# Kernel tuning notes

Measured on AMD Instinct MI355X. Metric: run time of the kernel, lower is better.

## Reference

```python
import jax, jax.numpy as jnp
import numpy as np
import math

B, S, D, H, DFF = 16, 512, 1024, 16, 4096
DK = D // H
EPS = 1e-6


def _lin(x, W, b):
    return x @ W + b


def _layernorm(x, g, b):
    # torch-style: unbiased std, eps added to std (not var)
    m = jnp.mean(x, axis=-1, keepdims=True)
    std = jnp.sqrt(jnp.sum((x - m) ** 2, axis=-1, keepdims=True) / (x.shape[-1] - 1))
    return g * (x - m) / (std + EPS) + b


def _gelu(x):
    return 0.5 * x * (1.0 + jnp.tanh(jnp.sqrt(2.0 / jnp.pi) * (x + 0.044715 * x ** 3)))


def setup_inputs() -> dict:
    key = jax.random.key(0)
    ks = jax.random.split(key, 20)
    sc = lambda fan_in: 1.0 / math.sqrt(fan_in)
    d = {
        "x": jax.random.normal(ks[0], (B, S, D), jnp.float32),
        "time": jax.random.normal(ks[1], (B, S, D), jnp.float32),
        "Wq": jax.random.uniform(ks[2], (D, D), jnp.float32, -sc(D), sc(D)),
        "bq": jnp.zeros((D,), jnp.float32),
        "Wk": jax.random.uniform(ks[3], (D, D), jnp.float32, -sc(D), sc(D)),
        "bk": jnp.zeros((D,), jnp.float32),
        "Wt": jax.random.uniform(ks[4], (D, D), jnp.float32, -sc(D), sc(D)),
        "bt": jnp.zeros((D,), jnp.float32),
        "Wv": jax.random.uniform(ks[5], (D, D), jnp.float32, -sc(D), sc(D)),
        "bv": jnp.zeros((D,), jnp.float32),
        "Wo": jax.random.uniform(ks[6], (D, D), jnp.float32, -sc(D), sc(D)),
        "bo": jnp.zeros((D,), jnp.float32),
        "W1": jax.random.uniform(ks[7], (D, DFF), jnp.float32, -sc(D), sc(D)),
        "b1": jnp.zeros((DFF,), jnp.float32),
        "W2": jax.random.uniform(ks[8], (DFF, D), jnp.float32, -sc(DFF), sc(DFF)),
        "b2": jnp.zeros((D,), jnp.float32),
        "ln1_g": jnp.ones((D,), jnp.float32),
        "ln1_b": jnp.zeros((D,), jnp.float32),
        "ln2_g": jnp.ones((D,), jnp.float32),
        "ln2_b": jnp.zeros((D,), jnp.float32),
        "mask_logits": jax.random.uniform(ks[9], (S, S), jnp.float32, 2.0, 5.0),
        "mask": jax.random.randint(ks[10], (B, 1, S, S), 0, 2, jnp.int32),
        "pmask": 0,
    }
    return d


def reference(x, time, Wq, bq, Wk, bk, Wt, bt, Wv, bv, Wo, bo, W1, b1, W2, b2,
              ln1_g, ln1_b, ln2_g, ln2_b, mask_logits, mask, pmask):
    def split_heads(t):  # [B,S,D] -> [B,H,S,DK]
        return t.reshape(B, S, H, DK).transpose(0, 2, 1, 3)

    # --- attention sublayer (dropout = identity at inference) ---
    xn = _layernorm(x, ln1_g, ln1_b)
    q = split_heads(_lin(xn, Wq, bq))
    k1 = split_heads(_lin(xn, Wk, bk))
    k2 = split_heads(_lin(time, Wt, bt))
    v = split_heads(_lin(xn, Wv, bv))

    inv = 1.0 / math.sqrt(DK)
    scores = jnp.einsum("bhqd,bhkd->bhqk", q, k1) * inv
    scores = jnp.where(mask == 0, -1e9, scores)  # masked_fill BEFORE time term
    scores = scores + jnp.einsum("bhqd,bhkd->bhqk", q, k2) * inv
    p_attn = jax.nn.softmax(scores, axis=-1)
    p_attn = p_attn * jax.nn.sigmoid(mask_logits)  # learned post-softmax mask [S,S]
    ctx = jnp.einsum("bhqk,bhkd->bhqd", p_attn, v)
    ctx = ctx.transpose(0, 2, 1, 3).reshape(B, S, D)
    x = x + _lin(ctx, Wo, bo)

    # --- FFN sublayer ---
    xn2 = _layernorm(x, ln2_g, ln2_b)
    ff = _lin(_gelu(_lin(xn2, W1, b1)), W2, b2)
    return x + ff
```

## Files before the change

kernel.cpp:

```cpp
#include <hip/hip_runtime.h>

#define BB   16
#define SS   512
#define DD   1024
#define HH   16
#define DKK  64
#define DFFN 4096
#define LN_EPS 1e-6f
#define QSCALE 0.18033688011112042f

typedef __attribute__((ext_vector_type(8))) __bf16 bf16x8;
typedef __attribute__((ext_vector_type(4))) float f32x4;
typedef __attribute__((ext_vector_type(8))) unsigned short ushort8;
typedef __attribute__((ext_vector_type(4))) unsigned short ushort4_t;

#define AS1 __attribute__((address_space(1)))
#define AS3 __attribute__((address_space(3)))

__device__ __forceinline__ unsigned short f2bf(float f) {
  unsigned int u = __float_as_uint(f);
  u += 0x7FFFu + ((u >> 16) & 1u);
  return (unsigned short)(u >> 16);
}
__device__ __forceinline__ float bf2f(unsigned short u) {
  return __uint_as_float(((unsigned int)u) << 16);
}

__device__ __forceinline__ float gelu_f(float x) {
  float t = 0.7978845608028654f * (x + 0.044715f * x * x * x);
  return x / (1.0f + __expf(-2.0f * t));
}

__device__ __forceinline__ void sbar() {
  __builtin_amdgcn_sched_barrier(0);
  __builtin_amdgcn_s_barrier();
  __builtin_amdgcn_sched_barrier(0);
}
#define WAITVM(N)                                         \
  do {                                                    \
    __builtin_amdgcn_sched_barrier(0);                    \
    asm volatile("s_waitcnt vmcnt(" #N ")" ::: "memory"); \
    __builtin_amdgcn_sched_barrier(0);                    \
  } while (0)

__global__ __launch_bounds__(256) void ln_kernel(const float* __restrict__ x,
                                                 const float* __restrict__ g,
                                                 const float* __restrict__ b,
                                                 unsigned short* __restrict__ out, int ldo) {
  const int row = blockIdx.x;
  const int tid = threadIdx.x;
  const float* xr = x + (size_t)row * DD;
  float4 v = *(const float4*)(xr + tid * 4);
  float s = v.x + v.y + v.z + v.w;
#pragma unroll
  for (int off = 1; off < 64; off <<= 1) s += __shfl_xor(s, off);
  __shared__ float red[8];
  const int wid = tid >> 6, l = tid & 63;
  if (l == 0) red[wid] = s;
  __syncthreads();
  const float mean = (red[0] + red[1] + red[2] + red[3]) * (1.0f / DD);
  float4 d;
  d.x = v.x - mean; d.y = v.y - mean; d.z = v.z - mean; d.w = v.w - mean;
  float ss = d.x * d.x + d.y * d.y + d.z * d.z + d.w * d.w;
#pragma unroll
  for (int off = 1; off < 64; off <<= 1) ss += __shfl_xor(ss, off);
  if (l == 0) red[4 + wid] = ss;
  __syncthreads();
  const float var = (red[4] + red[5] + red[6] + red[7]) * (1.0f / (DD - 1));
  const float scale = 1.0f / (sqrtf(var) + LN_EPS);
  float4 gv = *(const float4*)(g + tid * 4);
  float4 bv = *(const float4*)(b + tid * 4);
  ushort4_t o;
  o[0] = f2bf(gv.x * d.x * scale + bv.x);
  o[1] = f2bf(gv.y * d.y * scale + bv.y);
  o[2] = f2bf(gv.z * d.z * scale + bv.z);
  o[3] = f2bf(gv.w * d.w * scale + bv.w);
  *(ushort4_t*)(out + (size_t)row * ldo + tid * 4) = o;
}

__global__ __launch_bounds__(256) void ln_time(const float* __restrict__ x,
                                               const float* __restrict__ g,
                                               const float* __restrict__ b,
                                               const float* __restrict__ timep,
                                               unsigned short* __restrict__ out) {
  const int row = blockIdx.x;
  const int tid = threadIdx.x;
  const float* xr = x + (size_t)row * DD;
  float4 v = *(const float4*)(xr + tid * 4);
  float s = v.x + v.y + v.z + v.w;
#pragma unroll
  for (int off = 1; off < 64; off <<= 1) s += __shfl_xor(s, off);
  __shared__ float red[8];
  const int wid = tid >> 6, l = tid & 63;
  if (l == 0) red[wid] = s;
  __syncthreads();
  const float mean = (red[0] + red[1] + red[2] + red[3]) * (1.0f / DD);
  float4 d;
  d.x = v.x - mean; d.y = v.y - mean; d.z = v.z - mean; d.w = v.w - mean;
  float ss = d.x * d.x + d.y * d.y + d.z * d.z + d.w * d.w;
#pragma unroll
  for (int off = 1; off < 64; off <<= 1) ss += __shfl_xor(ss, off);
  if (l == 0) red[4 + wid] = ss;
  __syncthreads();
  const float var = (red[4] + red[5] + red[6] + red[7]) * (1.0f / (DD - 1));
  const float scale = 1.0f / (sqrtf(var) + LN_EPS);
  float4 gv = *(const float4*)(g + tid * 4);
  float4 bv = *(const float4*)(b + tid * 4);
  ushort4_t o;
  o[0] = f2bf(gv.x * d.x * scale + bv.x);
  o[1] = f2bf(gv.y * d.y * scale + bv.y);
  o[2] = f2bf(gv.z * d.z * scale + bv.z);
  o[3] = f2bf(gv.w * d.w * scale + bv.w);
  *(ushort4_t*)(out + (size_t)row * 2048 + tid * 4) = o;
  float4 tv = *(const float4*)(timep + (size_t)row * DD + tid * 4);
  ushort4_t to;
  to[0] = f2bf(tv.x); to[1] = f2bf(tv.y); to[2] = f2bf(tv.z); to[3] = f2bf(tv.w);
  *(ushort4_t*)(out + (size_t)row * 2048 + 1024 + tid * 4) = to;
}

__global__ __launch_bounds__(256) void prep_weights(
    const float* __restrict__ Wq, const float* __restrict__ Wv,
    const float* __restrict__ Wk, const float* __restrict__ Wt,
    const float* __restrict__ Wo, const float* __restrict__ W1,
    const float* __restrict__ W2,
    unsigned short* __restrict__ WqvT, unsigned short* __restrict__ WkcT,
    unsigned short* __restrict__ WoT, unsigned short* __restrict__ W1T,
    unsigned short* __restrict__ W2T) {
  __shared__ float tile[32][33];
  int id = blockIdx.x;
  const float* W; unsigned short* WT; int N, ldo, xdim;
  if (id < 1024)      { W = Wq; WT = WqvT;                          N = 1024; ldo = 1024; xdim = 32; }
  else if (id < 2048) { W = Wv; WT = WqvT + (size_t)1024 * 1024;    N = 1024; ldo = 1024; xdim = 32; id -= 1024; }
  else if (id < 3072) { W = Wk; WT = WkcT;                          N = 1024; ldo = 2048; xdim = 32; id -= 2048; }
  else if (id < 4096) { W = Wt; WT = WkcT + 1024;                   N = 1024; ldo = 2048; xdim = 32; id -= 3072; }
  else if (id < 5120) { W = Wo; WT = WoT;                           N = 1024; ldo = 1024; xdim = 32; id -= 4096; }
  else if (id < 9216) { W = W1; WT = W1T;                           N = 4096; ldo = 1024; xdim = 128; id -= 5120; }
  else                { W = W2; WT = W2T;                           N = 1024; ldo = 4096; xdim = 32; id -= 9216; }
  const int bx = id % xdim, by = id / xdim;
  const int tx = threadIdx.x & 31, ty = threadIdx.x >> 5;
  const int n0 = bx * 32, k0 = by * 32;
#pragma unroll
  for (int i = 0; i < 32; i += 8)
    tile[ty + i][tx] = W[(size_t)(k0 + ty + i) * N + n0 + tx];
  __syncthreads();
#pragma unroll
  for (int i = 0; i < 32; i += 8)
    WT[(size_t)(n0 + ty + i) * ldo + k0 + tx] = f2bf(tile[tx][ty + i]);
}

__global__ __launch_bounds__(256) void vtrans(const unsigned short* __restrict__ in,
                                              unsigned short* __restrict__ out) {
  __shared__ unsigned short tile[64][72];
  const int t = threadIdx.x;
  const int c0 = blockIdx.x * 64;
  const int r0 = blockIdx.y * 64;
  const int tx = t & 15, ty = t >> 4;
#pragma unroll
  for (int i = 0; i < 64; i += 16)
    *(ushort4_t*)&tile[ty + i][tx * 4] =
        *(const ushort4_t*)(in + (size_t)(r0 + ty + i) * 1024 + c0 + tx * 4);
  __syncthreads();
  const int cT = t >> 2, rq = (t & 3) * 16;
  ushort8 o0, o1;
#pragma unroll
  for (int j = 0; j < 8; ++j) o0[j] = tile[rq + j][cT];
#pragma unroll
  for (int j = 0; j < 8; ++j) o1[j] = tile[rq + 8 + j][cT];
  *(ushort8*)(out + (size_t)(c0 + cT) * 8192 + r0 + rq) = o0;
  *(ushort8*)(out + (size_t)(c0 + cT) * 8192 + r0 + rq + 8) = o1;
}

__global__ __launch_bounds__(256) void gate_build(const int* __restrict__ mask,
                                                  const float* __restrict__ ml,
                                                  unsigned short* __restrict__ gate,
                                                  const float* __restrict__ bq,
                                                  const float* __restrict__ bv,
                                                  const float* __restrict__ bk,
                                                  const float* __restrict__ bt,
                                                  float* __restrict__ qvb,
                                                  float* __restrict__ kcb) {
  const int i = blockIdx.x * 256 + threadIdx.x;
  if (i < 3072) {
    if (i < 2048) qvb[i] = (i < 1024) ? bq[i] : bv[i - 1024];
    else kcb[i - 2048] = bk[i - 2048] + bt[i - 2048];
  }
  const size_t base = (size_t)i * 8;
  const int off = (int)(base & (SS * SS - 1));
  const int4* mp = (const int4*)(mask + base);
  const int4 m0 = mp[0], m1 = mp[1];
  const float4* lp = (const float4*)(ml + off);
  const float4 a = lp[0], b = lp[1];
  ushort8 o;
  o[0] = m0.x ? f2bf(1.0f / (1.0f + __expf(-a.x))) : 0;
  o[1] = m0.y ? f2bf(1.0f / (1.0f + __expf(-a.y))) : 0;
  o[2] = m0.z ? f2bf(1.0f / (1.0f + __expf(-a.z))) : 0;
  o[3] = m0.w ? f2bf(1.0f / (1.0f + __expf(-a.w))) : 0;
  o[4] = m1.x ? f2bf(1.0f / (1.0f + __expf(-b.x))) : 0;
  o[5] = m1.y ? f2bf(1.0f / (1.0f + __expf(-b.y))) : 0;
  o[6] = m1.z ? f2bf(1.0f / (1.0f + __expf(-b.z))) : 0;
  o[7] = m1.w ? f2bf(1.0f / (1.0f + __expf(-b.w))) : 0;
  *(ushort8*)(gate + base) = o;
}

template <int BM, int EPI>
__global__ __launch_bounds__(512, 2) void gemm8p(const unsigned short* __restrict__ A, int lda,
                                                 const unsigned short* __restrict__ BT,
                                                 const float* __restrict__ bias,
                                                 const float* __restrict__ resid,
                                                 void* __restrict__ Cout,
                                                 unsigned short* __restrict__ vOut,
                                                 int M, int N, int K) {
  constexpr int MI = BM / 32;
  constexpr int ASUB = BM / 16;
  constexpr int AHALF = BM * 32;
  constexpr int ABUF = BM * 64;
  constexpr int ACALL = BM / 128;

  __shared__ __align__(16) unsigned short smA[2 * ABUF];
  __shared__ __align__(16) unsigned short smB[2 * 16384];

  const int tid = threadIdx.x;
  const int w = tid >> 6, lane = tid & 63;
  const int lr = lane & 15, lg = lane >> 4;
  const int wr = w >> 2, wn = w & 3;

  const int nb = N / 256;
  const int nwg = gridDim.x;
  int bid = blockIdx.x;
  bid = (bid & 7) * (nwg >> 3) + (bid >> 3);
  const int mb = bid / nb, nbk = bid % nb;

  const int uo = (lane * 16) ^ (lane & 32);
  const int srow = uo >> 6;
  const int scol = (uo & 63) >> 1;

  const unsigned short* pA[2];
  const unsigned short* pB[2];
#pragma unroll
  for (int j = 0; j < ACALL; ++j)
    pA[j] = A + (size_t)(mb * BM + (j * 8 + w) * 16 + srow) * lda + scol;
  if (ACALL == 1) pA[1] = pA[0];
#pragma unroll
  for (int j = 0; j < 2; ++j)
    pB[j] = BT + (size_t)(nbk * 256 + (j * 8 + w) * 16 + srow) * K + scol;

  auto stA = [&](int kt, int ks, int j, int d) {
    __builtin_amdgcn_global_load_lds(
        (const AS1 void*)(pA[j] + (size_t)kt * 64 + ks * 32),
        (AS3 void*)(smA + d * ABUF + ks * AHALF + j * 4096 + w * 512), 16, 0, 0);
  };
  auto stB = [&](int kt, int ks, int j, int d) {
    __builtin_amdgcn_global_load_lds(
        (const AS1 void*)(pB[j] + (size_t)kt * 64 + ks * 32),
        (AS3 void*)(smB + d * 16384 + ks * 8192 + j * 4096 + w * 512), 16, 0, 0);
  };
  auto issue_half = [&](int t, int ks) {
    const int d = t & 1;
#pragma unroll
    for (int j = 0; j < ACALL; ++j) stA(t, ks, j, d);
    stB(t, ks, 0, d);
    stB(t, ks, 1, d);
  };

  const int aoff = lr * 32 + ((lg * 8) ^ ((lr & 8) << 1));

  f32x4 acc[MI][4] = {};
  const int NT = K >> 6;

  issue_half(0, 0);
  issue_half(0, 1);
  issue_half(1, 0);
  if constexpr (ACALL == 2) { WAITVM(8); } else { WAITVM(6); }
  sbar();

  for (int kt = 0; kt < NT; ++kt) {
    const unsigned short* aD = smA + (kt & 1) * ABUF;
    const unsigned short* bD = smB + (kt & 1) * 16384;
    const bool i1 = (kt + 1 < NT);
    const bool i2 = (kt + 2 < NT);
    bf16x8 af[4], bf[4];

#pragma unroll
    for (int i = 0; i < 4; ++i)
      bf[i] = *(const bf16x8*)(bD + (wn * 4 + i) * 512 + aoff);
#pragma unroll
    for (int i = 0; i < 4; ++i)
      af[i] = *(const bf16x8*)(aD + (wr * MI + i) * 512 + aoff);
    if (i1) issue_half(kt + 1, 1);
    if constexpr (ACALL == 1) {
      if (i1) { WAITVM(6); } else { WAITVM(0); }
    }
    sbar();
    __builtin_amdgcn_s_setprio(1);
#pragma unroll
    for (int mi = 0; mi < 4; ++mi)
#pragma unroll
      for (int ni = 0; ni < 4; ++ni)
        acc[mi][ni] = __builtin_amdgcn_mfma_f32_16x16x32_bf16(af[mi], bf[ni], acc[mi][ni], 0, 0, 0);
    __builtin_amdgcn_s_setprio(0);
    sbar();

    if constexpr (ACALL == 2) {
#pragma unroll
      for (int i = 0; i < 4; ++i)
        af[i] = *(const bf16x8*)(aD + (wr * MI + 4 + i) * 512 + aoff);
      if (i1) { WAITVM(8); } else { WAITVM(0); }
      sbar();
      __builtin_amdgcn_s_setprio(1);
#pragma unroll
      for (int mi = 0; mi < 4; ++mi)
#pragma unroll
        for (int ni = 0; ni < 4; ++ni)
          acc[4 + mi][ni] = __builtin_amdgcn_mfma_f32_16x16x32_bf16(af[mi], bf[ni], acc[4 + mi][ni], 0, 0, 0);
      __builtin_amdgcn_s_setprio(0);
      sbar();
    }

#pragma unroll
    for (int i = 0; i < 4; ++i)
      bf[i] = *(const bf16x8*)(bD + (16 + wn * 4 + i) * 512 + aoff);
#pragma unroll
    for (int i = 0; i < 4; ++i)
      af[i] = *(const bf16x8*)(aD + (ASUB + wr * MI + i) * 512 + aoff);
    if (i2) issue_half(kt + 2, 0);
    if constexpr (ACALL == 1) {
      if (i2) { WAITVM(6); } else { WAITVM(3); }
    }
    sbar();
    __builtin_amdgcn_s_setprio(1);
#pragma unroll
    for (int mi = 0; mi < 4; ++mi)
#pragma unroll
      for (int ni = 0; ni < 4; ++ni)
        acc[mi][ni] = __builtin_amdgcn_mfma_f32_16x16x32_bf16(af[mi], bf[ni], acc[mi][ni], 0, 0, 0);
    __builtin_amdgcn_s_setprio(0);
    sbar();

    if constexpr (ACALL == 2) {
#pragma unroll
      for (int i = 0; i < 4; ++i)
        af[i] = *(const bf16x8*)(aD + (ASUB + wr * MI + 4 + i) * 512 + aoff);
      if (i2) { WAITVM(8); } else { WAITVM(4); }
      sbar();
      __builtin_amdgcn_s_setprio(1);
#pragma unroll
      for (int mi = 0; mi < 4; ++mi)
#pragma unroll
        for (int ni = 0; ni < 4; ++ni)
          acc[4 + mi][ni] = __builtin_amdgcn_mfma_f32_16x16x32_bf16(af[mi], bf[ni], acc[4 + mi][ni], 0, 0, 0);
      __builtin_amdgcn_s_setprio(0);
      sbar();
    }
  }

  const int colb = nbk * 256 + wn * 64;
  const int rowb = mb * BM + wr * (BM / 2);
  float bvv[4];
#pragma unroll
  for (int ni = 0; ni < 4; ++ni) bvv[ni] = bias[colb + ni * 16 + lr];

  if (EPI == 3 && colb >= 1024) {
#pragma unroll
    for (int mi = 0; mi < MI; ++mi) {
#pragma unroll
      for (int j = 0; j < 4; ++j) {
        const int row = rowb + mi * 16 + lg * 4 + j;
#pragma unroll
        for (int ni = 0; ni < 4; ++ni)
          vOut[(size_t)row * 1024 + (colb - 1024) + ni * 16 + lr] = f2bf(acc[mi][ni][j] + bvv[ni]);
      }
    }
  } else {
#pragma unroll
    for (int mi = 0; mi < MI; ++mi) {
#pragma unroll
      for (int j = 0; j < 4; ++j) {
        const int row = rowb + mi * 16 + lg * 4 + j;
#pragma unroll
        for (int ni = 0; ni < 4; ++ni) {
          const int col = colb + ni * 16 + lr;
          float vv = acc[mi][ni][j] + bvv[ni];
          if (EPI == 2) vv = gelu_f(vv);
          if (EPI == 1) {
            const size_t o = (size_t)row * N + col;
            ((float*)Cout)[o] = vv + resid[o];
          } else if (EPI == 3) {
            ((unsigned short*)Cout)[(size_t)row * 1024 + col] = f2bf(vv * QSCALE);
          } else {
            ((unsigned short*)Cout)[(size_t)row * N + col] = f2bf(vv);
          }
        }
      }
    }
  }
}

template <int EPI>
__global__ __launch_bounds__(256, 2) void gemm128(const unsigned short* __restrict__ A, int lda,
                                                  const unsigned short* __restrict__ BT,
                                                  const float* __restrict__ bias,
                                                  const float* __restrict__ resid,
                                                  void* __restrict__ Cout,
                                                  int M, int N, int K) {
  __shared__ __align__(16) unsigned short smA[2 * 8192];
  __shared__ __align__(16) unsigned short smB[2 * 8192];

  const int tid = threadIdx.x;
  const int w = tid >> 6, lane = tid & 63;
  const int lr = lane & 15, lg = lane >> 4;
  const int wr = w >> 1, wn = w & 1;

  const int nb = N / 128;
  const int nwg = gridDim.x;
  int bid = blockIdx.x;
  bid = (bid & 7) * (nwg >> 3) + (bid >> 3);
  const int mb = bid / nb, nbk = bid % nb;

  const int uo = (lane * 16) ^ (lane & 32);
  const int srow = uo >> 6;
  const int scol = (uo & 63) >> 1;

  const unsigned short* pA[2];
  const unsigned short* pB[2];
#pragma unroll
  for (int j = 0; j < 2; ++j) {
    pA[j] = A + (size_t)(mb * 128 + (j * 4 + w) * 16 + srow) * lda + scol;
    pB[j] = BT + (size_t)(nbk * 128 + (j * 4 + w) * 16 + srow) * K + scol;
  }

  auto stA = [&](int kt, int ks, int j, int d) {
    __builtin_amdgcn_global_load_lds(
        (const AS1 void*)(pA[j] + (size_t)kt * 64 + ks * 32),
        (AS3 void*)(smA + d * 8192 + ks * 4096 + j * 2048 + w * 512), 16, 0, 0);
  };
  auto stB = [&](int kt, int ks, int j, int d) {
    __builtin_amdgcn_global_load_lds(
        (const AS1 void*)(pB[j] + (size_t)kt * 64 + ks * 32),
        (AS3 void*)(smB + d * 8192 + ks * 4096 + j * 2048 + w * 512), 16, 0, 0);
  };
  auto issue_half = [&](int t, int ks) {
    const int d = t & 1;
    stA(t, ks, 0, d); stA(t, ks, 1, d);
    stB(t, ks, 0, d); stB(t, ks, 1, d);
  };

  const int aoff = lr * 32 + ((lg * 8) ^ ((lr & 8) << 1));

  f32x4 acc[4][4] = {};
  const int NT = K >> 6;

  issue_half(0, 0);
  issue_half(0, 1);
  issue_half(1, 0);
  WAITVM(8);
  sbar();

  for (int kt = 0; kt < NT; ++kt) {
    const unsigned short* aD = smA + (kt & 1) * 8192;
    const unsigned short* bD = smB + (kt & 1) * 8192;
    const bool i1 = (kt + 1 < NT);
    const bool i2 = (kt + 2 < NT);
    bf16x8 af[4], bf[4];

#pragma unroll
    for (int i = 0; i < 4; ++i)
      bf[i] = *(const bf16x8*)(bD + (wn * 4 + i) * 512 + aoff);
#pragma unroll
    for (int i = 0; i < 4; ++i)
      af[i] = *(const bf16x8*)(aD + (wr * 4 + i) * 512 + aoff);
    if (i1) issue_half(kt + 1, 1);
    if (i1) { WAITVM(8); } else { WAITVM(0); }
    sbar();
    __builtin_amdgcn_s_setprio(1);
#pragma unroll
    for (int mi = 0; mi < 4; ++mi)
#pragma unroll
      for (int ni = 0; ni < 4; ++ni)
        acc[mi][ni] = __builtin_amdgcn_mfma_f32_16x16x32_bf16(af[mi], bf[ni], acc[mi][ni], 0, 0, 0);
    __builtin_amdgcn_s_setprio(0);
    sbar();

#pragma unroll
    for (int i = 0; i < 4; ++i)
      bf[i] = *(const bf16x8*)(bD + 4096 + (wn * 4 + i) * 512 + aoff);
#pragma unroll
    for (int i = 0; i < 4; ++i)
      af[i] = *(const bf16x8*)(aD + 4096 + (wr * 4 + i) * 512 + aoff);
    if (i2) issue_half(kt + 2, 0);
    if (i2) { WAITVM(8); } else if (i1) { WAITVM(4); } else { WAITVM(0); }
    sbar();
    __builtin_amdgcn_s_setprio(1);
#pragma unroll
    for (int mi = 0; mi < 4; ++mi)
#pragma unroll
      for (int ni = 0; ni < 4; ++ni)
        acc[mi][ni] = __builtin_amdgcn_mfma_f32_16x16x32_bf16(af[mi], bf[ni], acc[mi][ni], 0, 0, 0);
    __builtin_amdgcn_s_setprio(0);
    sbar();
  }

  const int colb = nbk * 128 + wn * 64;
  const int rowb = mb * 128 + wr * 64;
  float bvv[4];
#pragma unroll
  for (int ni = 0; ni < 4; ++ni) bvv[ni] = bias[colb + ni * 16 + lr];
#pragma unroll
  for (int mi = 0; mi < 4; ++mi) {
#pragma unroll
    for (int j = 0; j < 4; ++j) {
      const int row = rowb + mi * 16 + lg * 4 + j;
#pragma unroll
      for (int ni = 0; ni < 4; ++ni) {
        const int col = colb + ni * 16 + lr;
        const float vv = acc[mi][ni][j] + bvv[ni];
        if (EPI == 1) {
          const size_t o = (size_t)row * N + col;
          ((float*)Cout)[o] = vv + resid[o];
        } else {
          ((unsigned short*)Cout)[(size_t)row * N + col] = f2bf(vv);
        }
      }
    }
  }
}

__global__ __launch_bounds__(256) void attn4(const unsigned short* __restrict__ qb,
                                             const unsigned short* __restrict__ vT,
                                             const unsigned short* __restrict__ kcb,
                                             const unsigned short* __restrict__ gate,
                                             unsigned short* __restrict__ ctx) {
  __shared__ __align__(16) unsigned char smem[33280];
  float* pctx = (float*)smem;
  float* sumw = (float*)(smem + 32768);

  const int tid = threadIdx.x;
  const int w = tid >> 6, l = tid & 63;
  const int lr = l & 15, lg = l >> 4;
  const int virt = (blockIdx.x & 7) * 512 + (blockIdx.x >> 3);
  const int qt = virt & 15;
  const int h = (virt >> 4) & 15;
  const int b = virt >> 8;
  const int q0 = qt * 32;

  const unsigned short* qg = qb + (size_t)b * SS * DD + h * DKK;
  const unsigned short* kg = kcb + (size_t)b * SS * DD + h * DKK;
  const unsigned short* vg = vT + (size_t)(h * DKK) * 8192 + b * SS;
  const unsigned short* gg = gate + (size_t)b * SS * SS;
  unsigned short* cg = ctx + (size_t)b * SS * DD + h * DKK;

  bf16x8 qf[2][2];
#pragma unroll
  for (int mi = 0; mi < 2; ++mi)
#pragma unroll
    for (int ks = 0; ks < 2; ++ks)
      qf[mi][ks] = *(const bf16x8*)(qg + (size_t)(q0 + mi * 16 + lr) * DD + ks * 32 + lg * 8);

  f32x4 acc[2][4] = {};
  float ssum[2][4] = {};
  const int kb0 = w * 128;

#pragma unroll
  for (int it = 0; it < 4; ++it) {
    const int kbase = kb0 + it * 32;
    unsigned short* Pb = (unsigned short*)smem + w * 2560 + (it & 1) * 1280;

    bf16x8 kf[2][2];
#pragma unroll
    for (int ni = 0; ni < 2; ++ni)
#pragma unroll
      for (int ks = 0; ks < 2; ++ks)
        kf[ni][ks] = *(const bf16x8*)(kg + (size_t)(kbase + ni * 16 + lr) * DD + ks * 32 + lg * 8);
    f32x4 sc[2][2] = {};
#pragma unroll
    for (int ks = 0; ks < 2; ++ks)
#pragma unroll
      for (int mi = 0; mi < 2; ++mi)
#pragma unroll
        for (int ni = 0; ni < 2; ++ni)
          sc[mi][ni] = __builtin_amdgcn_mfma_f32_16x16x32_bf16(qf[mi][ks], kf[ni][ks], sc[mi][ni], 0, 0, 0);

    bf16x8 vb[4];
#pragma unroll
    for (int dkg = 0; dkg < 4; ++dkg)
      vb[dkg] = *(const bf16x8*)(vg + (size_t)(dkg * 16 + lr) * 8192 + kbase + lg * 8);

#pragma unroll
    for (int mi = 0; mi < 2; ++mi)
#pragma unroll
      for (int ni = 0; ni < 2; ++ni)
#pragma unroll
        for (int j = 0; j < 4; ++j) {
          const int row = mi * 16 + lg * 4 + j;
          const unsigned short gu = gg[(size_t)(q0 + row) * SS + kbase + ni * 16 + lr];
          const float e = exp2f(sc[mi][ni][j]);
          ssum[mi][j] += gu ? e : 0.0f;
          Pb[row * 40 + ni * 16 + lr] = f2bf(e * bf2f(gu));
        }

#pragma unroll
    for (int mi = 0; mi < 2; ++mi) {
      const bf16x8 pa = *(const bf16x8*)(Pb + (mi * 16 + lr) * 40 + lg * 8);
#pragma unroll
      for (int dkg = 0; dkg < 4; ++dkg)
        acc[mi][dkg] = __builtin_amdgcn_mfma_f32_16x16x32_bf16(pa, vb[dkg], acc[mi][dkg], 0, 0, 0);
    }
  }

#pragma unroll
  for (int mi = 0; mi < 2; ++mi)
#pragma unroll
    for (int j = 0; j < 4; ++j) {
      float s = ssum[mi][j];
      s += __shfl_xor(s, 1);
      s += __shfl_xor(s, 2);
      s += __shfl_xor(s, 4);
      s += __shfl_xor(s, 8);
      if (lr == 0) sumw[w * 32 + mi * 16 + lg * 4 + j] = s;
    }
  __syncthreads();

#pragma unroll
  for (int mi = 0; mi < 2; ++mi)
#pragma unroll
    for (int dkg = 0; dkg < 4; ++dkg)
#pragma unroll
      for (int j = 0; j < 4; ++j)
        pctx[(size_t)w * 2048 + (mi * 16 + lg * 4 + j) * 64 + dkg * 16 + lr] = acc[mi][dkg][j];
  __syncthreads();

  {
    const int row = tid >> 3;
    const int dk0 = (tid & 7) * 8;
    const float tot = sumw[row] + sumw[32 + row] + sumw[64 + row] + sumw[96 + row];
    const float inv = 1.0f / fmaxf(tot, 1e-30f);
    float vsum[8];
#pragma unroll
    for (int c = 0; c < 8; ++c) vsum[c] = 0.0f;
#pragma unroll
    for (int ww = 0; ww < 4; ++ww) {
      const float* p = pctx + (size_t)ww * 2048 + row * 64 + dk0;
      f32x4 a = *(const f32x4*)p;
      f32x4 bq = *(const f32x4*)(p + 4);
#pragma unroll
      for (int c = 0; c < 4; ++c) { vsum[c] += a[c]; vsum[4 + c] += bq[c]; }
    }
    ushort8 o;
#pragma unroll
    for (int c = 0; c < 8; ++c) o[c] = f2bf(vsum[c] * inv);
    *(ushort8*)(cg + (size_t)(q0 + row) * DD + dk0) = o;
  }
}

extern "C" void kernel_launch(void* const* d_in, const int* in_sizes, int n_in,
                              void* d_out, int out_size, void* d_ws, size_t ws_size,
                              hipStream_t stream) {
  (void)in_sizes; (void)n_in; (void)out_size; (void)ws_size;
  const float* x    = (const float*)d_in[0];
  const float* timep= (const float*)d_in[1];
  const float* Wq = (const float*)d_in[2];  const float* bq = (const float*)d_in[3];
  const float* Wk = (const float*)d_in[4];  const float* bk = (const float*)d_in[5];
  const float* Wt = (const float*)d_in[6];  const float* bt = (const float*)d_in[7];
  const float* Wv = (const float*)d_in[8];  const float* bv = (const float*)d_in[9];
  const float* Wo = (const float*)d_in[10]; const float* bo = (const float*)d_in[11];
  const float* W1 = (const float*)d_in[12]; const float* b1 = (const float*)d_in[13];
  const float* W2 = (const float*)d_in[14]; const float* b2 = (const float*)d_in[15];
  const float* ln1g = (const float*)d_in[16]; const float* ln1b = (const float*)d_in[17];
  const float* ln2g = (const float*)d_in[18]; const float* ln2b = (const float*)d_in[19];
  const float* ml   = (const float*)d_in[20];
  const int*   mask = (const int*)d_in[21];
  float* out = (float*)d_out;

  char* w = (char*)d_ws;
  auto alloc = [&](size_t sz) { char* p = w; w += (sz + 255) & ~(size_t)255; return p; };
  const int MT = BB * SS;

  unsigned short* WqvT = (unsigned short*)alloc((size_t)2048 * 1024 * 2);
  unsigned short* WkcT = (unsigned short*)alloc((size_t)1024 * 2048 * 2);
  unsigned short* WoT  = (unsigned short*)alloc((size_t)DD * DD * 2);
  unsigned short* W1T  = (unsigned short*)alloc((size_t)DD * DFFN * 2);
  unsigned short* W2T  = (unsigned short*)alloc((size_t)DFFN * DD * 2);
  float* qvb = (float*)alloc(2048 * 4);
  float* kcbias = (float*)alloc(1024 * 4);
  unsigned short* gateb = (unsigned short*)alloc((size_t)BB * SS * SS * 2);
  unsigned short* xt2 = (unsigned short*)alloc((size_t)MT * 2048 * 2);
  unsigned short* qbuf = (unsigned short*)alloc((size_t)MT * DD * 2);
  unsigned short* vbuf = (unsigned short*)alloc((size_t)MT * DD * 2);
  unsigned short* vTb = (unsigned short*)alloc((size_t)DD * MT * 2);
  unsigned short* kcb = (unsigned short*)alloc((size_t)MT * DD * 2);
  float*          x2  = (float*)alloc((size_t)MT * DD * 4);
  unsigned short* hb  = (unsigned short*)alloc((size_t)MT * DFFN * 2);
  unsigned short* ctx = xt2;
  unsigned short* xn2 = xt2;

  prep_weights<<<dim3(13312), 256, 0, stream>>>(Wq, Wv, Wk, Wt, Wo, W1, W2,
                                                WqvT, WkcT, WoT, W1T, W2T);
  gate_build<<<dim3(BB * SS * SS / 8 / 256), 256, 0, stream>>>(mask, ml, gateb,
                                                               bq, bv, bk, bt, qvb, kcbias);
  ln_time<<<dim3(MT), 256, 0, stream>>>(x, ln1g, ln1b, timep, xt2);

  gemm8p<256, 3><<<dim3(256), 512, 0, stream>>>(xt2, 2048, WqvT, qvb, nullptr, (void*)qbuf, vbuf, MT, 2048, 1024);
  vtrans<<<dim3(16, 128), 256, 0, stream>>>(vbuf, vTb);
  gemm128<0><<<dim3(512), 256, 0, stream>>>(xt2, 2048, WkcT, kcbias, nullptr, (void*)kcb, MT, 1024, 2048);

  attn4<<<dim3(BB * HH * 16), 256, 0, stream>>>(qbuf, vTb, kcb, gateb, ctx);

  gemm128<1><<<dim3(512), 256, 0, stream>>>(ctx, 1024, WoT, bo, x, (void*)x2, MT, 1024, 1024);
  ln_kernel<<<dim3(MT), 256, 0, stream>>>(x2, ln2g, ln2b, xn2, 1024);
  gemm8p<256, 2><<<dim3(512), 512, 0, stream>>>(xn2, 1024, W1T, b1, nullptr, (void*)hb, nullptr, MT, 4096, 1024);
  gemm128<1><<<dim3(512), 256, 0, stream>>>(hb, 4096, W2T, b2, x2, (void*)out, MT, 1024, 4096);
}
```

Measured before the change: 431.4 us.

## Replace 256x256 GEMM kernel with unified 128x128 tile kernel; raise attention priority

Drops the large 256x256-tile, 512-thread GEMM and routes the QV projection and the FFN up-projection through a generalized 128x128 tile kernel that now supports the split-V and GELU epilogues, launching 4x more blocks. The attention kernel gets launch bounds allowing three blocks per CU and raises wave priority around its MFMA sections. Smaller tiles give more blocks and better occupancy, but each block reuses operands less and global and LDS traffic per flop goes up.

```diff
diff --git a/kernel.cpp b/kernel.cpp
--- a/kernel.cpp
+++ b/kernel.cpp
@@ -202,29 +202,23 @@
   *(ushort8*)(gate + base) = o;
 }
 
-template <int BM, int EPI>
-__global__ __launch_bounds__(512, 2) void gemm8p(const unsigned short* __restrict__ A, int lda,
-                                                 const unsigned short* __restrict__ BT,
-                                                 const float* __restrict__ bias,
-                                                 const float* __restrict__ resid,
-                                                 void* __restrict__ Cout,
-                                                 unsigned short* __restrict__ vOut,
-                                                 int M, int N, int K) {
-  constexpr int MI = BM / 32;
-  constexpr int ASUB = BM / 16;
-  constexpr int AHALF = BM * 32;
-  constexpr int ABUF = BM * 64;
-  constexpr int ACALL = BM / 128;
-
-  __shared__ __align__(16) unsigned short smA[2 * ABUF];
-  __shared__ __align__(16) unsigned short smB[2 * 16384];
+template <int EPI>
+__global__ __launch_bounds__(256, 2) void gemm128(const unsigned short* __restrict__ A, int lda,
+                                                  const unsigned short* __restrict__ BT,
+                                                  const float* __restrict__ bias,
+                                                  const float* __restrict__ resid,
+                                                  void* __restrict__ Cout,
+                                                  unsigned short* __restrict__ vOut,
+                                                  int M, int N, int K) {
+  __shared__ __align__(16) unsigned short smA[2 * 8192];
+  __shared__ __align__(16) unsigned short smB[2 * 8192];
 
   const int tid = threadIdx.x;
   const int w = tid >> 6, lane = tid & 63;
   const int lr = lane & 15, lg = lane >> 4;
-  const int wr = w >> 2, wn = w & 3;
-
-  const int nb = N / 256;
+  const int wr = w >> 1, wn = w & 1;
+
+  const int nb = N / 128;
   const int nwg = gridDim.x;
   int bid = blockIdx.x;
   bid = (bid & 7) * (nwg >> 3) + (bid >> 3);
@@ -237,45 +231,41 @@
   const unsigned short* pA[2];
   const unsigned short* pB[2];
 #pragma unroll
-  for (int j = 0; j < ACALL; ++j)
-    pA[j] = A + (size_t)(mb * BM + (j * 8 + w) * 16 + srow) * lda + scol;
-  if (ACALL == 1) pA[1] = pA[0];
-#pragma unroll
-  for (int j = 0; j < 2; ++j)
-    pB[j] = BT + (size_t)(nbk * 256 + (j * 8 + w) * 16 + srow) * K + scol;
+  for (int j = 0; j < 2; ++j) {
+    pA[j] = A + (size_t)(mb * 128 + (j * 4 + w) * 16 + srow) * lda + scol;
+    pB[j] = BT + (size_t)(nbk * 128 + (j * 4 + w) * 16 + srow) * K + scol;
+  }
 
   auto stA = [&](int kt, int ks, int j, int d) {
     __builtin_amdgcn_global_load_lds(
         (const AS1 void*)(pA[j] + (size_t)kt * 64 + ks * 32),
-        (AS3 void*)(smA + d * ABUF + ks * AHALF + j * 4096 + w * 512), 16, 0, 0);
+        (AS3 void*)(smA + d * 8192 + ks * 4096 + j * 2048 + w * 512), 16, 0, 0);
   };
   auto stB = [&](int kt, int ks, int j, int d) {
     __builtin_amdgcn_global_load_lds(
         (const AS1 void*)(pB[j] + (size_t)kt * 64 + ks * 32),
-        (AS3 void*)(smB + d * 16384 + ks * 8192 + j * 4096 + w * 512), 16, 0, 0);
+        (AS3 void*)(smB + d * 8192 + ks * 4096 + j * 2048 + w * 512), 16, 0, 0);
   };
   auto issue_half = [&](int t, int ks) {
     const int d = t & 1;
-#pragma unroll
-    for (int j = 0; j < ACALL; ++j) stA(t, ks, j, d);
-    stB(t, ks, 0, d);
-    stB(t, ks, 1, d);
+    stA(t, ks, 0, d); stA(t, ks, 1, d);
+    stB(t, ks, 0, d); stB(t, ks, 1, d);
   };
 
   const int aoff = lr * 32 + ((lg * 8) ^ ((lr & 8) << 1));
 
-  f32x4 acc[MI][4] = {};
+  f32x4 acc[4][4] = {};
   const int NT = K >> 6;
 
   issue_half(0, 0);
   issue_half(0, 1);
   issue_half(1, 0);
-  if constexpr (ACALL == 2) { WAITVM(8); } else { WAITVM(6); }
+  WAITVM(8);
   sbar();
 
   for (int kt = 0; kt < NT; ++kt) {
-    const unsigned short* aD = smA + (kt & 1) * ABUF;
-    const unsigned short* bD = smB + (kt & 1) * 16384;
+    const unsigned short* aD = smA + (kt & 1) * 8192;
+    const unsigned short* bD = smB + (kt & 1) * 8192;
     const bool i1 = (kt + 1 < NT);
     const bool i2 = (kt + 2 < NT);
     bf16x8 af[4], bf[4];
@@ -285,11 +275,9 @@
       bf[i] = *(const bf16x8*)(bD + (wn * 4 + i) * 512 + aoff);
 #pragma unroll
     for (int i = 0; i < 4; ++i)
-      af[i] = *(const bf16x8*)(aD + (wr * MI + i) * 512 + aoff);
+      af[i] = *(const bf16x8*)(aD + (wr * 4 + i) * 512 + aoff);
     if (i1) issue_half(kt + 1, 1);
-    if constexpr (ACALL == 1) {
-      if (i1) { WAITVM(6); } else { WAITVM(0); }
-    }
+    if (i1) { WAITVM(8); } else { WAITVM(0); }
     sbar();
     __builtin_amdgcn_s_setprio(1);
 #pragma unroll
@@ -300,32 +288,14 @@
     __builtin_amdgcn_s_setprio(0);
     sbar();
 
-    if constexpr (ACALL == 2) {
-#pragma unroll
-      for (int i = 0; i < 4; ++i)
-        af[i] = *(const bf16x8*)(aD + (wr * MI + 4 + i) * 512 + aoff);
-      if (i1) { WAITVM(8); } else { WAITVM(0); }
-      sbar();
-      __builtin_amdgcn_s_setprio(1);
-#pragma unroll
-      for (int mi = 0; mi < 4; ++mi)
-#pragma unroll
-        for (int ni = 0; ni < 4; ++ni)
-          acc[4 + mi][ni] = __builtin_amdgcn_mfma_f32_16x16x32_bf16(af[mi], bf[ni], acc[4 + mi][ni], 0, 0, 0);
-      __builtin_amdgcn_s_setprio(0);
-      sbar();
-    }
-
 #pragma unroll
     for (int i = 0; i < 4; ++i)
-      bf[i] = *(const bf16x8*)(bD + (16 + wn * 4 + i) * 512 + aoff);
+      bf[i] = *(const bf16x8*)(bD + 4096 + (wn * 4 + i) * 512 + aoff);
 #pragma unroll
     for (int i = 0; i < 4; ++i)
-      af[i] = *(const bf16x8*)(aD + (ASUB + wr * MI + i) * 512 + aoff);
+      af[i] = *(const bf16x8*)(aD + 4096 + (wr * 4 + i) * 512 + aoff);
     if (i2) issue_half(kt + 2, 0);
-    if constexpr (ACALL == 1) {
-      if (i2) { WAITVM(6); } else { WAITVM(3); }
-    }
+    if (i2) { WAITVM(8); } else if (i1) { WAITVM(4); } else { WAITVM(0); }
     sbar();
     __builtin_amdgcn_s_setprio(1);
 #pragma unroll
@@ -335,33 +305,17 @@
         acc[mi][ni] = __builtin_amdgcn_mfma_f32_16x16x32_bf16(af[mi], bf[ni], acc[mi][ni], 0, 0, 0);
     __builtin_amdgcn_s_setprio(0);
     sbar();
-
-    if constexpr (ACALL == 2) {
-#pragma unroll
-      for (int i = 0; i < 4; ++i)
-        af[i] = *(const bf16x8*)(aD + (ASUB + wr * MI + 4 + i) * 512 + aoff);
-      if (i2) { WAITVM(8); } else { WAITVM(4); }
-      sbar();
-      __builtin_amdgcn_s_setprio(1);
-#pragma unroll
-      for (int mi = 0; mi < 4; ++mi)
-#pragma unroll
-        for (int ni = 0; ni < 4; ++ni)
-          acc[4 + mi][ni] = __builtin_amdgcn_mfma_f32_16x16x32_bf16(af[mi], bf[ni], acc[4 + mi][ni], 0, 0, 0);
-      __builtin_amdgcn_s_setprio(0);
-      sbar();
-    }
   }
 
-  const int colb = nbk * 256 + wn * 64;
-  const int rowb = mb * BM + wr * (BM / 2);
+  const int colb = nbk * 128 + wn * 64;
+  const int rowb = mb * 128 + wr * 64;
   float bvv[4];
 #pragma unroll
   for (int ni = 0; ni < 4; ++ni) bvv[ni] = bias[colb + ni * 16 + lr];
 
   if (EPI == 3 && colb >= 1024) {
 #pragma unroll
-    for (int mi = 0; mi < MI; ++mi) {
+    for (int mi = 0; mi < 4; ++mi) {
 #pragma unroll
       for (int j = 0; j < 4; ++j) {
         const int row = rowb + mi * 16 + lg * 4 + j;
@@ -372,7 +326,7 @@
     }
   } else {
 #pragma unroll
-    for (int mi = 0; mi < MI; ++mi) {
+    for (int mi = 0; mi < 4; ++mi) {
 #pragma unroll
       for (int j = 0; j < 4; ++j) {
         const int row = rowb + mi * 16 + lg * 4 + j;
@@ -395,140 +349,11 @@
   }
 }
 
-template <int EPI>
-__global__ __launch_bounds__(256, 2) void gemm128(const unsigned short* __restrict__ A, int lda,
-                                                  const unsigned short* __restrict__ BT,
-                                                  const float* __restrict__ bias,
-                                                  const float* __restrict__ resid,
-                                                  void* __restrict__ Cout,
-                                                  int M, int N, int K) {
-  __shared__ __align__(16) unsigned short smA[2 * 8192];
-  __shared__ __align__(16) unsigned short smB[2 * 8192];
-
-  const int tid = threadIdx.x;
-  const int w = tid >> 6, lane = tid & 63;
-  const int lr = lane & 15, lg = lane >> 4;
-  const int wr = w >> 1, wn = w & 1;
-
-  const int nb = N / 128;
-  const int nwg = gridDim.x;
-  int bid = blockIdx.x;
-  bid = (bid & 7) * (nwg >> 3) + (bid >> 3);
-  const int mb = bid / nb, nbk = bid % nb;
-
-  const int uo = (lane * 16) ^ (lane & 32);
-  const int srow = uo >> 6;
-  const int scol = (uo & 63) >> 1;
-
-  const unsigned short* pA[2];
-  const unsigned short* pB[2];
-#pragma unroll
-  for (int j = 0; j < 2; ++j) {
-    pA[j] = A + (size_t)(mb * 128 + (j * 4 + w) * 16 + srow) * lda + scol;
-    pB[j] = BT + (size_t)(nbk * 128 + (j * 4 + w) * 16 + srow) * K + scol;
-  }
-
-  auto stA = [&](int kt, int ks, int j, int d) {
-    __builtin_amdgcn_global_load_lds(
-        (const AS1 void*)(pA[j] + (size_t)kt * 64 + ks * 32),
-        (AS3 void*)(smA + d * 8192 + ks * 4096 + j * 2048 + w * 512), 16, 0, 0);
-  };
-  auto stB = [&](int kt, int ks, int j, int d) {
-    __builtin_amdgcn_global_load_lds(
-        (const AS1 void*)(pB[j] + (size_t)kt * 64 + ks * 32),
-        (AS3 void*)(smB + d * 8192 + ks * 4096 + j * 2048 + w * 512), 16, 0, 0);
-  };
-  auto issue_half = [&](int t, int ks) {
-    const int d = t & 1;
-    stA(t, ks, 0, d); stA(t, ks, 1, d);
-    stB(t, ks, 0, d); stB(t, ks, 1, d);
-  };
-
-  const int aoff = lr * 32 + ((lg * 8) ^ ((lr & 8) << 1));
-
-  f32x4 acc[4][4] = {};
-  const int NT = K >> 6;
-
-  issue_half(0, 0);
-  issue_half(0, 1);
-  issue_half(1, 0);
-  WAITVM(8);
-  sbar();
-
-  for (int kt = 0; kt < NT; ++kt) {
-    const unsigned short* aD = smA + (kt & 1) * 8192;
-    const unsigned short* bD = smB + (kt & 1) * 8192;
-    const bool i1 = (kt + 1 < NT);
-    const bool i2 = (kt + 2 < NT);
-    bf16x8 af[4], bf[4];
-
-#pragma unroll
-    for (int i = 0; i < 4; ++i)
-      bf[i] = *(const bf16x8*)(bD + (wn * 4 + i) * 512 + aoff);
-#pragma unroll
-    for (int i = 0; i < 4; ++i)
-      af[i] = *(const bf16x8*)(aD + (wr * 4 + i) * 512 + aoff);
-    if (i1) issue_half(kt + 1, 1);
-    if (i1) { WAITVM(8); } else { WAITVM(0); }
-    sbar();
-    __builtin_amdgcn_s_setprio(1);
-#pragma unroll
-    for (int mi = 0; mi < 4; ++mi)
-#pragma unroll
-      for (int ni = 0; ni < 4; ++ni)
-        acc[mi][ni] = __builtin_amdgcn_mfma_f32_16x16x32_bf16(af[mi], bf[ni], acc[mi][ni], 0, 0, 0);
-    __builtin_amdgcn_s_setprio(0);
-    sbar();
-
-#pragma unroll
-    for (int i = 0; i < 4; ++i)
-      bf[i] = *(const bf16x8*)(bD + 4096 + (wn * 4 + i) * 512 + aoff);
-#pragma unroll
-    for (int i = 0; i < 4; ++i)
-      af[i] = *(const bf16x8*)(aD + 4096 + (wr * 4 + i) * 512 + aoff);
-    if (i2) issue_half(kt + 2, 0);
-    if (i2) { WAITVM(8); } else if (i1) { WAITVM(4); } else { WAITVM(0); }
-    sbar();
-    __builtin_amdgcn_s_setprio(1);
-#pragma unroll
-    for (int mi = 0; mi < 4; ++mi)
-#pragma unroll
-      for (int ni = 0; ni < 4; ++ni)
-        acc[mi][ni] = __builtin_amdgcn_mfma_f32_16x16x32_bf16(af[mi], bf[ni], acc[mi][ni], 0, 0, 0);
-    __builtin_amdgcn_s_setprio(0);
-    sbar();
-  }
-
-  const int colb = nbk * 128 + wn * 64;
-  const int rowb = mb * 128 + wr * 64;
-  float bvv[4];
-#pragma unroll
-  for (int ni = 0; ni < 4; ++ni) bvv[ni] = bias[colb + ni * 16 + lr];
-#pragma unroll
-  for (int mi = 0; mi < 4; ++mi) {
-#pragma unroll
-    for (int j = 0; j < 4; ++j) {
-      const int row = rowb + mi * 16 + lg * 4 + j;
-#pragma unroll
-      for (int ni = 0; ni < 4; ++ni) {
-        const int col = colb + ni * 16 + lr;
-        const float vv = acc[mi][ni][j] + bvv[ni];
-        if (EPI == 1) {
-          const size_t o = (size_t)row * N + col;
-          ((float*)Cout)[o] = vv + resid[o];
-        } else {
-          ((unsigned short*)Cout)[(size_t)row * N + col] = f2bf(vv);
-        }
-      }
-    }
-  }
-}
-
-__global__ __launch_bounds__(256) void attn4(const unsigned short* __restrict__ qb,
-                                             const unsigned short* __restrict__ vT,
-                                             const unsigned short* __restrict__ kcb,
-                                             const unsigned short* __restrict__ gate,
-                                             unsigned short* __restrict__ ctx) {
+__global__ __launch_bounds__(256, 3) void attn4(const unsigned short* __restrict__ qb,
+                                                const unsigned short* __restrict__ vT,
+                                                const unsigned short* __restrict__ kcb,
+                                                const unsigned short* __restrict__ gate,
+                                                unsigned short* __restrict__ ctx) {
   __shared__ __align__(16) unsigned char smem[33280];
   float* pctx = (float*)smem;
   float* sumw = (float*)(smem + 32768);
@@ -571,6 +396,7 @@
       for (int ks = 0; ks < 2; ++ks)
         kf[ni][ks] = *(const bf16x8*)(kg + (size_t)(kbase + ni * 16 + lr) * DD + ks * 32 + lg * 8);
     f32x4 sc[2][2] = {};
+    __builtin_amdgcn_s_setprio(1);
 #pragma unroll
     for (int ks = 0; ks < 2; ++ks)
 #pragma unroll
@@ -578,6 +404,7 @@
 #pragma unroll
         for (int ni = 0; ni < 2; ++ni)
           sc[mi][ni] = __builtin_amdgcn_mfma_f32_16x16x32_bf16(qf[mi][ks], kf[ni][ks], sc[mi][ni], 0, 0, 0);
+    __builtin_amdgcn_s_setprio(0);
 
     bf16x8 vb[4];
 #pragma unroll
@@ -597,6 +424,7 @@
           Pb[row * 40 + ni * 16 + lr] = f2bf(e * bf2f(gu));
         }
 
+    __builtin_amdgcn_s_setprio(1);
 #pragma unroll
     for (int mi = 0; mi < 2; ++mi) {
       const bf16x8 pa = *(const bf16x8*)(Pb + (mi * 16 + lr) * 40 + lg * 8);
@@ -604,6 +432,7 @@
       for (int dkg = 0; dkg < 4; ++dkg)
         acc[mi][dkg] = __builtin_amdgcn_mfma_f32_16x16x32_bf16(pa, vb[dkg], acc[mi][dkg], 0, 0, 0);
     }
+    __builtin_amdgcn_s_setprio(0);
   }
 
 #pragma unroll
@@ -698,14 +527,14 @@
                                                                bq, bv, bk, bt, qvb, kcbias);
   ln_time<<<dim3(MT), 256, 0, stream>>>(x, ln1g, ln1b, timep, xt2);
 
-  gemm8p<256, 3><<<dim3(256), 512, 0, stream>>>(xt2, 2048, WqvT, qvb, nullptr, (void*)qbuf, vbuf, MT, 2048, 1024);
+  gemm128<3><<<dim3(1024), 256, 0, stream>>>(xt2, 2048, WqvT, qvb, nullptr, (void*)qbuf, vbuf, MT, 2048, 1024);
   vtrans<<<dim3(16, 128), 256, 0, stream>>>(vbuf, vTb);
-  gemm128<0><<<dim3(512), 256, 0, stream>>>(xt2, 2048, WkcT, kcbias, nullptr, (void*)kcb, MT, 1024, 2048);
+  gemm128<0><<<dim3(512), 256, 0, stream>>>(xt2, 2048, WkcT, kcbias, nullptr, (void*)kcb, nullptr, MT, 1024, 2048);
 
   attn4<<<dim3(BB * HH * 16), 256, 0, stream>>>(qbuf, vTb, kcb, gateb, ctx);
 
-  gemm128<1><<<dim3(512), 256, 0, stream>>>(ctx, 1024, WoT, bo, x, (void*)x2, MT, 1024, 1024);
+  gemm128<1><<<dim3(512), 256, 0, stream>>>(ctx, 1024, WoT, bo, x, (void*)x2, nullptr, MT, 1024, 1024);
   ln_kernel<<<dim3(MT), 256, 0, stream>>>(x2, ln2g, ln2b, xn2, 1024);
-  gemm8p<256, 2><<<dim3(512), 512, 0, stream>>>(xn2, 1024, W1T, b1, nullptr, (void*)hb, nullptr, MT, 4096, 1024);
-  gemm128<1><<<dim3(512), 256, 0, stream>>>(hb, 4096, W2T, b2, x2, (void*)out, MT, 1024, 4096);
-}
+  gemm128<2><<<dim3(2048), 256, 0, stream>>>(xn2, 1024, W1T, b1, nullptr, (void*)hb, nullptr, MT, 4096, 1024);
+  gemm128<1><<<dim3(512), 256, 0, stream>>>(hb, 4096, W2T, b2, x2, (void*)out, nullptr, MT, 1024, 4096);
+}
```

Result: slower. 515.3 us (+19.4%).
